# Performance work log

Measured on AMD Instinct MI355X. Metric: run time of the kernel, lower is better.

## Reference

```python
import jax, jax.numpy as jnp
import numpy as np

N_NODES = 100000
N_EDGES = 1600000
D_IN, D_HID, D_OUT = 128, 128, 40


def _degrees(src, dst, n):
    ones = jnp.ones((src.shape[0],), dtype=jnp.float32)
    out_deg = jax.ops.segment_sum(ones, src, num_segments=n)
    in_deg = jax.ops.segment_sum(ones, dst, num_segments=n)
    # DGL clamps zero degrees to 1 to avoid inf
    return jnp.maximum(out_deg, 1.0), jnp.maximum(in_deg, 1.0)


def _graph_conv(x, W, b, src, dst, out_norm, in_norm, n):
    # norm='both': h = D_in^{-1/2} * A^T * (D_out^{-1/2} * x W) + b
    h = x @ W                      # [N, d_out] (W applied first: d_in >= d_out)
    h = h * out_norm[:, None]      # scale source features
    agg = jax.ops.segment_sum(h[src], dst, num_segments=n)  # gather-scatter SpMM
    return agg * in_norm[:, None] + b


def setup_inputs() -> dict:
    key = jax.random.key(0)
    ks = jax.random.split(key, 8)
    x = jax.random.normal(ks[0], (N_NODES, D_IN), dtype=jnp.float32)
    edge_index = jax.random.randint(ks[1], (2, N_EDGES), 0, N_NODES, dtype=jnp.int32)
    def glorot(k, fan_in, fan_out):
        lim = np.sqrt(6.0 / (fan_in + fan_out)).astype(np.float32)
        return jax.random.uniform(k, (fan_in, fan_out), jnp.float32, -lim, lim)
    return {
        "x": x,
        "edge_index": edge_index,
        "W1": glorot(ks[2], D_IN, D_HID), "b1": jnp.zeros((D_HID,), jnp.float32),
        "W2": glorot(ks[3], D_HID, D_HID), "b2": jnp.zeros((D_HID,), jnp.float32),
        "W3": glorot(ks[4], D_HID, D_OUT), "b3": jnp.zeros((D_OUT,), jnp.float32),
    }


def reference(x, edge_index, W1, b1, W2, b2, W3, b3):
    src, dst = edge_index[0], edge_index[1]
    out_deg, in_deg = _degrees(src, dst, N_NODES)
    out_norm = jax.lax.rsqrt(out_deg)
    in_norm = jax.lax.rsqrt(in_deg)
    h = _graph_conv(x, W1, b1, src, dst, out_norm, in_norm, N_NODES)
    h = jax.nn.relu(h)  # dropout inactive at inference
    h = _graph_conv(h, W2, b2, src, dst, out_norm, in_norm, N_NODES)
    h = jax.nn.relu(h)
    h = _graph_conv(h, W3, b3, src, dst, out_norm, in_norm, N_NODES)
    return jax.nn.log_softmax(h, axis=-1)
```

## Files before the change

### kernel.cpp

```cpp
#include <hip/hip_runtime.h>
#include <hip/hip_bf16.h>
#include <math.h>

typedef __hip_bfloat16 bf16;
typedef __attribute__((ext_vector_type(8))) short short8v;
typedef __attribute__((ext_vector_type(4))) float f32x4;

#define ELLW 64
#define NPB 256
#define NBMAX 512
#define CAPB 8192
#define CHUNKA 4096

__device__ __forceinline__ float bflo(unsigned u) { return __uint_as_float(u << 16); }
__device__ __forceinline__ float bfhi(unsigned u) { return __uint_as_float(u & 0xffff0000u); }
__device__ __forceinline__ unsigned short f2bf(float f) {
    unsigned u = __float_as_uint(f);
    return (unsigned short)((u + 0x7fff + ((u >> 16) & 1)) >> 16);
}


__global__ void bucket_scatter(const int* __restrict__ src, const int* __restrict__ dst,
                               int nbk, int* __restrict__ gCurD, int* __restrict__ gCurS,
                               unsigned* __restrict__ pairD, int* __restrict__ srcS, int E) {
    __shared__ int histD[NBMAX], histS[NBMAX], offD[NBMAX], offS[NBMAX];
    int tid = threadIdx.x;
    int base = blockIdx.x * CHUNKA;
    int cnt = E - base; if (cnt > CHUNKA) cnt = CHUNKA;
    for (int i = tid; i < nbk; i += 256) { histD[i] = 0; histS[i] = 0; }
    __syncthreads();
    int sv[16], dv[16];
#pragma unroll
    for (int j = 0; j < 16; ++j) {
        int idx = tid + j * 256;
        if (idx < cnt) {
            sv[j] = src[base + idx];
            dv[j] = dst[base + idx];
            atomicAdd(&histD[dv[j] >> 8], 1);
            atomicAdd(&histS[sv[j] >> 8], 1);
        } else sv[j] = -1;
    }
    __syncthreads();
    for (int i = tid; i < nbk; i += 256) {
        offD[i] = atomicAdd(&gCurD[i], histD[i]);
        offS[i] = atomicAdd(&gCurS[i], histS[i]);
    }
    __syncthreads();
    for (int i = tid; i < nbk; i += 256) { histD[i] = 0; histS[i] = 0; }
    __syncthreads();
#pragma unroll
    for (int j = 0; j < 16; ++j) {
        if (sv[j] >= 0) {
            int bd = dv[j] >> 8;
            int p = atomicAdd(&histD[bd], 1) + offD[bd];
            if (p < CAPB)
                pairD[(size_t)bd * CAPB + p] = ((unsigned)(dv[j] & 255) << 17) | (unsigned)sv[j];
            int bs = sv[j] >> 8;
            int q = atomicAdd(&histS[bs], 1) + offS[bs];
            if (q < CAPB) srcS[(size_t)bs * CAPB + q] = sv[j];
        }
    }
}

__global__ void norm_kernel(const int* __restrict__ cnt_out, const int* __restrict__ cnt_in,
                            float* __restrict__ outn, float* __restrict__ innf, int n) {
    int i = blockIdx.x * blockDim.x + threadIdx.x;
    if (i < n) {
        outn[i] = rsqrtf(fmaxf((float)cnt_out[i], 1.0f));
        innf[i] = rsqrtf(fmaxf((float)cnt_in[i], 1.0f));
    }
}


__device__ __forceinline__ void pack_one(const float* __restrict__ W, bf16* __restrict__ Wb,
                                         int idx, int NOUT, int NPAD) {
    int r = idx & 7;
    int rest = idx >> 3;
    int col = rest % NPAD;
    int sk = rest / NPAD;
    int k = sk * 8 + r;
    float v = (col < NOUT) ? W[k * NOUT + col] : 0.0f;
    Wb[idx] = __float2bfloat16(v);
}

__global__ void pack_all(const float* __restrict__ W1, const float* __restrict__ W2,
                         const float* __restrict__ W3, bf16* __restrict__ Wb1,
                         bf16* __restrict__ Wb2, bf16* __restrict__ Wb3) {
    int idx = blockIdx.x * blockDim.x + threadIdx.x;
    if (idx < 16384) pack_one(W1, Wb1, idx, 128, 128);
    else if (idx < 32768) pack_one(W2, Wb2, idx - 16384, 128, 128);
    else if (idx < 40960) pack_one(W3, Wb3, idx - 32768, 40, 64);
}


template <int NT>
__device__ void gemm_body_f32(int bid, const float* __restrict__ Af,
                              const bf16* __restrict__ Wb, bf16* __restrict__ H, int n) {
    constexpr int NPAD = NT * 16;
    int lane = threadIdx.x & 63;
    int wid = threadIdx.x >> 6;
    int base = (bid * 4 + wid) * 16;
    if (base >= n) return;
    int m = lane & 15, kb = lane >> 4;
    int arow = base + m;

    short8v az = {0, 0, 0, 0, 0, 0, 0, 0};
    short8v a[4];
    const float4* apf = (const float4*)(Af + (size_t)arow * 128);
#pragma unroll
    for (int s = 0; s < 4; ++s) {
        short8v w = az;
        if (arow < n) {
            float4 p = apf[s * 8 + kb * 2];
            float4 q = apf[s * 8 + kb * 2 + 1];
            w[0] = (short)f2bf(p.x); w[1] = (short)f2bf(p.y);
            w[2] = (short)f2bf(p.z); w[3] = (short)f2bf(p.w);
            w[4] = (short)f2bf(q.x); w[5] = (short)f2bf(q.y);
            w[6] = (short)f2bf(q.z); w[7] = (short)f2bf(q.w);
        }
        a[s] = w;
    }

    f32x4 zz = {0.f, 0.f, 0.f, 0.f};
    f32x4 acc[NT];
#pragma unroll
    for (int t = 0; t < NT; ++t) acc[t] = zz;

    const short8v* bp = (const short8v*)Wb;
#pragma unroll
    for (int s = 0; s < 4; ++s) {
#pragma unroll
        for (int t = 0; t < NT; ++t) {
            short8v b = bp[(size_t)(s * 4 + kb) * NPAD + t * 16 + m];
            acc[t] = __builtin_amdgcn_mfma_f32_16x16x32_bf16(a[s], b, acc[t], 0, 0, 0);
        }
    }

    int orow0 = base + kb * 4;
#pragma unroll
    for (int r = 0; r < 4; ++r) {
        int rr = orow0 + r;
        if (rr < n) {
#pragma unroll
            for (int t = 0; t < NT; ++t)
                H[(size_t)rr * NPAD + t * 16 + m] = __float2bfloat16(acc[t][r]);
        }
    }
}


__global__ void phase2(const unsigned* __restrict__ pairD, const int* __restrict__ srcS,
                       const int* __restrict__ gCurD, const int* __restrict__ gCurS,
                       int* __restrict__ ell, int* __restrict__ cnt_in, int* __restrict__ cnt_out,
                       int nbk, int n,
                       const float* __restrict__ x, const bf16* __restrict__ Wb1,
                       bf16* __restrict__ H) {
    int bid = blockIdx.x;
    int tid = threadIdx.x;
    if (bid < nbk) {
        __shared__ int cnt[NPB];
        cnt[tid & (NPB - 1)] = 0;
        __syncthreads();
        int m = gCurD[bid]; if (m > CAPB) m = CAPB;
        const unsigned* p = pairD + (size_t)bid * CAPB;
        int nb0 = bid << 8;
        for (int i = tid; i < m; i += 256) {
            unsigned v = p[i];
            int local = (int)(v >> 17);
            int s = (int)(v & 0x1FFFF);
            int pos = atomicAdd(&cnt[local], 1);
            if (pos < ELLW) ell[((size_t)(nb0 + local) << 6) + pos] = s;
        }
        __syncthreads();
        int node = nb0 + tid;
        if (tid < NPB && node < n) cnt_in[node] = cnt[tid];
    } else if (bid < 2 * nbk) {
        int b = bid - nbk;
        __shared__ int cnt2[NPB];
        cnt2[tid & (NPB - 1)] = 0;
        __syncthreads();
        int m = gCurS[b]; if (m > CAPB) m = CAPB;
        const int* p = srcS + (size_t)b * CAPB;
        int nb0 = b << 8;
        for (int i = tid; i < m; i += 256)
            atomicAdd(&cnt2[p[i] - nb0], 1);
        __syncthreads();
        int node = nb0 + tid;
        if (tid < NPB && node < n) cnt_out[node] = cnt2[tid];
    } else {
        gemm_body_f32<8>(bid - 2 * nbk, x, Wb1, H, n);
    }
}


template <int NT>
__global__ void gather_gemm_fused(const bf16* __restrict__ h, const int* __restrict__ cnt_in,
                                  const int* __restrict__ ell, const float* __restrict__ outn,
                                  const float* __restrict__ inn, const float* __restrict__ bias,
                                  const bf16* __restrict__ Wb, bf16* __restrict__ H, int n) {
    constexpr int NPAD = NT * 16;
    constexpr int NTW = NT / 4;
    __shared__ short rows[16][136];
    int lane = threadIdx.x & 63;
    int wid = threadIdx.x >> 6;
    int nodeBase = blockIdx.x * 16;
    const unsigned* hu = (const unsigned*)h;

#pragma unroll
    for (int q = 0; q < 4; ++q) {
        int r = wid * 4 + q;
        int node = nodeBase + r;
        unsigned pk = 0;
        if (node < n) {
            int d = min(cnt_in[node], ELLW);
            const int* row = ell + (size_t)node * ELLW;
            float a0 = 0.f, a1 = 0.f, a2 = 0.f, a3 = 0.f;
            float a4 = 0.f, a5 = 0.f, a6 = 0.f, a7 = 0.f;
            int k = 0;
            for (; k + 7 < d; k += 8) {
                int e0 = row[k],     e1 = row[k + 1], e2 = row[k + 2], e3 = row[k + 3];
                int e4 = row[k + 4], e5 = row[k + 5], e6 = row[k + 6], e7 = row[k + 7];
                unsigned u0 = hu[(size_t)e0 * 64 + lane];
                unsigned u1 = hu[(size_t)e1 * 64 + lane];
                unsigned u2 = hu[(size_t)e2 * 64 + lane];
                unsigned u3 = hu[(size_t)e3 * 64 + lane];
                unsigned u4 = hu[(size_t)e4 * 64 + lane];
                unsigned u5 = hu[(size_t)e5 * 64 + lane];
                unsigned u6 = hu[(size_t)e6 * 64 + lane];
                unsigned u7 = hu[(size_t)e7 * 64 + lane];
                float o0 = outn[e0], o1 = outn[e1], o2 = outn[e2], o3 = outn[e3];
                float o4 = outn[e4], o5 = outn[e5], o6 = outn[e6], o7 = outn[e7];
                a0 += o0 * bflo(u0); a1 += o0 * bfhi(u0);
                a2 += o1 * bflo(u1); a3 += o1 * bfhi(u1);
                a4 += o2 * bflo(u2); a5 += o2 * bfhi(u2);
                a6 += o3 * bflo(u3); a7 += o3 * bfhi(u3);
                a0 += o4 * bflo(u4); a1 += o4 * bfhi(u4);
                a2 += o5 * bflo(u5); a3 += o5 * bfhi(u5);
                a4 += o6 * bflo(u6); a5 += o6 * bfhi(u6);
                a6 += o7 * bflo(u7); a7 += o7 * bfhi(u7);
            }
            for (; k + 3 < d; k += 4) {
                int e0 = row[k], e1 = row[k + 1], e2 = row[k + 2], e3 = row[k + 3];
                unsigned u0 = hu[(size_t)e0 * 64 + lane];
                unsigned u1 = hu[(size_t)e1 * 64 + lane];
                unsigned u2 = hu[(size_t)e2 * 64 + lane];
                unsigned u3 = hu[(size_t)e3 * 64 + lane];
                float o0 = outn[e0], o1 = outn[e1], o2 = outn[e2], o3 = outn[e3];
                a0 += o0 * bflo(u0); a1 += o0 * bfhi(u0);
                a2 += o1 * bflo(u1); a3 += o1 * bfhi(u1);
                a4 += o2 * bflo(u2); a5 += o2 * bfhi(u2);
                a6 += o3 * bflo(u3); a7 += o3 * bfhi(u3);
            }
            for (; k < d; ++k) {
                int e = row[k];
                unsigned u = hu[(size_t)e * 64 + lane];
                float o = outn[e];
                a0 += o * bflo(u); a1 += o * bfhi(u);
            }
            float innv = inn[node];
            float2 bb = ((const float2*)bias)[lane];
            float f0 = fmaxf(((a0 + a2) + (a4 + a6)) * innv + bb.x, 0.0f);
            float f1 = fmaxf(((a1 + a3) + (a5 + a7)) * innv + bb.y, 0.0f);
            pk = (unsigned)f2bf(f0) | ((unsigned)f2bf(f1) << 16);
        }
        ((unsigned*)rows[r])[lane] = pk;
    }
    __syncthreads();

    int m = lane & 15, kb = lane >> 4;
    short8v a[4];
#pragma unroll
    for (int s = 0; s < 4; ++s)
        a[s] = *(const short8v*)&rows[m][s * 32 + kb * 8];

    f32x4 zz = {0.f, 0.f, 0.f, 0.f};
    f32x4 acc[NTW];
#pragma unroll
    for (int t = 0; t < NTW; ++t) acc[t] = zz;

    const short8v* bp = (const short8v*)Wb;
#pragma unroll
    for (int s = 0; s < 4; ++s) {
#pragma unroll
        for (int t = 0; t < NTW; ++t) {
            int tt = wid * NTW + t;
            short8v b = bp[(size_t)(s * 4 + kb) * NPAD + tt * 16 + m];
            acc[t] = __builtin_amdgcn_mfma_f32_16x16x32_bf16(a[s], b, acc[t], 0, 0, 0);
        }
    }

    int orow0 = nodeBase + kb * 4;
#pragma unroll
    for (int r = 0; r < 4; ++r) {
        int rr = orow0 + r;
        if (rr < n) {
#pragma unroll
            for (int t = 0; t < NTW; ++t)
                H[(size_t)rr * NPAD + (wid * NTW + t) * 16 + m] = __float2bfloat16(acc[t][r]);
        }
    }
}


__global__ void gather40_lsm_p64(const bf16* __restrict__ h, const int* __restrict__ cnt_in,
                                 const int* __restrict__ ell, const float* __restrict__ outn,
                                 const float* __restrict__ inn, const float* __restrict__ b,
                                 float* __restrict__ out, int n) {
    int node = blockIdx.x * 4 + (threadIdx.x >> 6);
    int lane = threadIdx.x & 63;
    if (node >= n) return;
    int d = min(cnt_in[node], ELLW);
    const int* row = ell + (size_t)node * ELLW;
    int grp = lane >> 5;
    int l = lane & 31;
    const unsigned* hu = (const unsigned*)h;
    float a0 = 0.f, a1 = 0.f, a2 = 0.f, a3 = 0.f;
    int k = grp;
    for (; k + 6 < d; k += 8) {
        int e0 = row[k], e1 = row[k + 2], e2 = row[k + 4], e3 = row[k + 6];
        unsigned u0 = hu[(size_t)e0 * 32 + l];
        unsigned u1 = hu[(size_t)e1 * 32 + l];
        unsigned u2 = hu[(size_t)e2 * 32 + l];
        unsigned u3 = hu[(size_t)e3 * 32 + l];
        float o0 = outn[e0], o1 = outn[e1], o2 = outn[e2], o3 = outn[e3];
        a0 += o0 * bflo(u0); a1 += o0 * bfhi(u0);
        a2 += o1 * bflo(u1); a3 += o1 * bfhi(u1);
        a0 += o2 * bflo(u2); a1 += o2 * bfhi(u2);
        a2 += o3 * bflo(u3); a3 += o3 * bfhi(u3);
    }
    for (; k + 2 < d; k += 4) {
        int e0 = row[k], e1 = row[k + 2];
        unsigned u0 = hu[(size_t)e0 * 32 + l];
        unsigned u1 = hu[(size_t)e1 * 32 + l];
        float o0 = outn[e0], o1 = outn[e1];
        a0 += o0 * bflo(u0); a1 += o0 * bfhi(u0);
        a2 += o1 * bflo(u1); a3 += o1 * bfhi(u1);
    }
    if (k < d) {
        int e = row[k];
        unsigned u = hu[(size_t)e * 32 + l];
        float o = outn[e];
        a0 += o * bflo(u); a1 += o * bfhi(u);
    }
    a0 += a2; a1 += a3;
    a0 += __shfl_xor(a0, 32);
    a1 += __shfl_xor(a1, 32);
    float innv = inn[node];
    bool act = (l < 20);
    float2 bb = act ? ((const float2*)b)[l] : make_float2(0.f, 0.f);
    float v0 = act ? (a0 * innv + bb.x) : -INFINITY;
    float v1 = act ? (a1 * innv + bb.y) : -INFINITY;
    float m = fmaxf(v0, v1);
#pragma unroll
    for (int o = 16; o; o >>= 1) m = fmaxf(m, __shfl_xor(m, o));
    float e = act ? (expf(v0 - m) + expf(v1 - m)) : 0.0f;
#pragma unroll
    for (int o = 16; o; o >>= 1) e += __shfl_xor(e, o);
    float ls = m + logf(e);
    if (act && grp == 0)
        ((float2*)(out + (size_t)node * 40))[l] = make_float2(v0 - ls, v1 - ls);
}


extern "C" void kernel_launch(void* const* d_in, const int* in_sizes, int n_in,
                              void* d_out, int out_size, void* d_ws, size_t ws_size,
                              hipStream_t stream) {
    const float* x  = (const float*)d_in[0];
    const int*   ei = (const int*)d_in[1];
    const float* W1 = (const float*)d_in[2];
    const float* b1 = (const float*)d_in[3];
    const float* W2 = (const float*)d_in[4];
    const float* b2 = (const float*)d_in[5];
    const float* W3 = (const float*)d_in[6];
    const float* b3 = (const float*)d_in[7];

    const int n = in_sizes[0] / 128;
    const int E = in_sizes[1] / 2;
    const int* src = ei;
    const int* dst = ei + E;
    const int nbk = (n + NPB - 1) / NPB;

    char* wsb = (char*)d_ws;
    size_t off = 0;
    auto alloc = [&](size_t bytes) { void* p = wsb + off; off = (off + bytes + 63) & ~(size_t)63; return p; };
    float*    outn    = (float*)alloc((size_t)n * 4);
    float*    innf    = (float*)alloc((size_t)n * 4);
    int*      cnt_out = (int*)alloc((size_t)n * 4);
    int*      cnt_in  = (int*)alloc((size_t)n * 4);
    int*      gCurD   = (int*)alloc((size_t)nbk * 4);
    int*      gCurS   = (int*)alloc((size_t)nbk * 4);
    int*      ell     = (int*)alloc((size_t)n * ELLW * 4);
    unsigned* pairD   = (unsigned*)alloc((size_t)nbk * CAPB * 4);
    bf16*     Wb1     = (bf16*)alloc(16 * 128 * 8 * 2);
    bf16*     Wb2     = (bf16*)alloc(16 * 128 * 8 * 2);
    bf16*     Wb3     = (bf16*)alloc(16 * 64 * 8 * 2);
    bf16*     hb      = (bf16*)alloc((size_t)n * 128 * 2);
    bf16*     gb      = (bf16*)alloc((size_t)n * 128 * 2);
    int*      srcS    = (int*)gb;

    hipMemsetAsync(gCurD, 0, ((size_t)((char*)gCurS - (char*)gCurD) + (size_t)nbk * 4), stream);

    pack_all<<<(40960 + 255) / 256, 256, 0, stream>>>(W1, W2, W3, Wb1, Wb2, Wb3);

    bucket_scatter<<<(E + CHUNKA - 1) / CHUNKA, 256, 0, stream>>>(src, dst, nbk, gCurD, gCurS,
                                                                  pairD, srcS, E);
    const int gemmBlocks = (n + 63) / 64;
    phase2<<<2 * nbk + gemmBlocks, 256, 0, stream>>>(pairD, srcS, gCurD, gCurS, ell, cnt_in,
                                                     cnt_out, nbk, n, x, Wb1, hb);
    norm_kernel<<<(n + 255) / 256, 256, 0, stream>>>(cnt_out, cnt_in, outn, innf, n);

    const int fblk = (n + 15) / 16;
    gather_gemm_fused<8><<<fblk, 256, 0, stream>>>(hb, cnt_in, ell, outn, innf, b1, Wb2, gb, n);
    gather_gemm_fused<4><<<fblk, 256, 0, stream>>>(gb, cnt_in, ell, outn, innf, b2, Wb3, hb, n);
    gather40_lsm_p64<<<(n + 3) / 4, 256, 0, stream>>>(hb, cnt_in, ell, outn, innf, b3,
                                                      (float*)d_out, n);
}
```

Measured before the change: 277.0 us.

## Fuse scatter with layer-1 GEMM, fold norm into phase2, widen gather unroll

The edge bucket scatter now runs in the same launch as the first dense GEMM, so the two independent jobs overlap, and the degree normalisation is computed directly in phase2, which removes the separate norm kernel and the cnt_out buffer. The gather loops in the fused gather-GEMM kernel now read neighbour indices as int4 and process 16 neighbours per iteration. The final 40-wide gather gets an extra 16-step unrolled loop. These changes cut launch count and raise memory-level parallelism, at the cost of higher register pressure from the wider unrolling.

```diff
diff --git a/kernel.cpp b/kernel.cpp
--- a/kernel.cpp
+++ b/kernel.cpp
@@ -17,58 +17,6 @@
 __device__ __forceinline__ unsigned short f2bf(float f) {
     unsigned u = __float_as_uint(f);
     return (unsigned short)((u + 0x7fff + ((u >> 16) & 1)) >> 16);
-}
-
-
-__global__ void bucket_scatter(const int* __restrict__ src, const int* __restrict__ dst,
-                               int nbk, int* __restrict__ gCurD, int* __restrict__ gCurS,
-                               unsigned* __restrict__ pairD, int* __restrict__ srcS, int E) {
-    __shared__ int histD[NBMAX], histS[NBMAX], offD[NBMAX], offS[NBMAX];
-    int tid = threadIdx.x;
-    int base = blockIdx.x * CHUNKA;
-    int cnt = E - base; if (cnt > CHUNKA) cnt = CHUNKA;
-    for (int i = tid; i < nbk; i += 256) { histD[i] = 0; histS[i] = 0; }
-    __syncthreads();
-    int sv[16], dv[16];
-#pragma unroll
-    for (int j = 0; j < 16; ++j) {
-        int idx = tid + j * 256;
-        if (idx < cnt) {
-            sv[j] = src[base + idx];
-            dv[j] = dst[base + idx];
-            atomicAdd(&histD[dv[j] >> 8], 1);
-            atomicAdd(&histS[sv[j] >> 8], 1);
-        } else sv[j] = -1;
-    }
-    __syncthreads();
-    for (int i = tid; i < nbk; i += 256) {
-        offD[i] = atomicAdd(&gCurD[i], histD[i]);
-        offS[i] = atomicAdd(&gCurS[i], histS[i]);
-    }
-    __syncthreads();
-    for (int i = tid; i < nbk; i += 256) { histD[i] = 0; histS[i] = 0; }
-    __syncthreads();
-#pragma unroll
-    for (int j = 0; j < 16; ++j) {
-        if (sv[j] >= 0) {
-            int bd = dv[j] >> 8;
-            int p = atomicAdd(&histD[bd], 1) + offD[bd];
-            if (p < CAPB)
-                pairD[(size_t)bd * CAPB + p] = ((unsigned)(dv[j] & 255) << 17) | (unsigned)sv[j];
-            int bs = sv[j] >> 8;
-            int q = atomicAdd(&histS[bs], 1) + offS[bs];
-            if (q < CAPB) srcS[(size_t)bs * CAPB + q] = sv[j];
-        }
-    }
-}
-
-__global__ void norm_kernel(const int* __restrict__ cnt_out, const int* __restrict__ cnt_in,
-                            float* __restrict__ outn, float* __restrict__ innf, int n) {
-    int i = blockIdx.x * blockDim.x + threadIdx.x;
-    if (i < n) {
-        outn[i] = rsqrtf(fmaxf((float)cnt_out[i], 1.0f));
-        innf[i] = rsqrtf(fmaxf((float)cnt_in[i], 1.0f));
-    }
 }
 
 
@@ -149,12 +97,65 @@
 }
 
 
+__device__ void scatter_body(int bid, const int* __restrict__ src, const int* __restrict__ dst,
+                             int nbk, int* __restrict__ gCurD, int* __restrict__ gCurS,
+                             unsigned* __restrict__ pairD, int* __restrict__ srcS, int E) {
+    __shared__ int histD[NBMAX], histS[NBMAX], offD[NBMAX], offS[NBMAX];
+    int tid = threadIdx.x;
+    int base = bid * CHUNKA;
+    int cnt = E - base; if (cnt > CHUNKA) cnt = CHUNKA;
+    for (int i = tid; i < nbk; i += 256) { histD[i] = 0; histS[i] = 0; }
+    __syncthreads();
+    int sv[16], dv[16];
+#pragma unroll
+    for (int j = 0; j < 16; ++j) {
+        int idx = tid + j * 256;
+        if (idx < cnt) {
+            sv[j] = src[base + idx];
+            dv[j] = dst[base + idx];
+            atomicAdd(&histD[dv[j] >> 8], 1);
+            atomicAdd(&histS[sv[j] >> 8], 1);
+        } else sv[j] = -1;
+    }
+    __syncthreads();
+    for (int i = tid; i < nbk; i += 256) {
+        offD[i] = atomicAdd(&gCurD[i], histD[i]);
+        offS[i] = atomicAdd(&gCurS[i], histS[i]);
+    }
+    __syncthreads();
+    for (int i = tid; i < nbk; i += 256) { histD[i] = 0; histS[i] = 0; }
+    __syncthreads();
+#pragma unroll
+    for (int j = 0; j < 16; ++j) {
+        if (sv[j] >= 0) {
+            int bd = dv[j] >> 8;
+            int p = atomicAdd(&histD[bd], 1) + offD[bd];
+            if (p < CAPB)
+                pairD[(size_t)bd * CAPB + p] = ((unsigned)(dv[j] & 255) << 17) | (unsigned)sv[j];
+            int bs = sv[j] >> 8;
+            int q = atomicAdd(&histS[bs], 1) + offS[bs];
+            if (q < CAPB) srcS[(size_t)bs * CAPB + q] = sv[j];
+        }
+    }
+}
+
+
+__global__ void phase1(const int* __restrict__ src, const int* __restrict__ dst,
+                       int nbk, int* __restrict__ gCurD, int* __restrict__ gCurS,
+                       unsigned* __restrict__ pairD, int* __restrict__ srcS, int E,
+                       int scatterBlocks, const float* __restrict__ x,
+                       const bf16* __restrict__ Wb1, bf16* __restrict__ H, int n) {
+    if ((int)blockIdx.x < scatterBlocks)
+        scatter_body(blockIdx.x, src, dst, nbk, gCurD, gCurS, pairD, srcS, E);
+    else
+        gemm_body_f32<8>(blockIdx.x - scatterBlocks, x, Wb1, H, n);
+}
+
+
 __global__ void phase2(const unsigned* __restrict__ pairD, const int* __restrict__ srcS,
                        const int* __restrict__ gCurD, const int* __restrict__ gCurS,
-                       int* __restrict__ ell, int* __restrict__ cnt_in, int* __restrict__ cnt_out,
-                       int nbk, int n,
-                       const float* __restrict__ x, const bf16* __restrict__ Wb1,
-                       bf16* __restrict__ H) {
+                       int* __restrict__ ell, int* __restrict__ cnt_in,
+                       float* __restrict__ innf, float* __restrict__ outn, int nbk, int n) {
     int bid = blockIdx.x;
     int tid = threadIdx.x;
     if (bid < nbk) {
@@ -173,8 +174,11 @@
         }
         __syncthreads();
         int node = nb0 + tid;
-        if (tid < NPB && node < n) cnt_in[node] = cnt[tid];
-    } else if (bid < 2 * nbk) {
+        if (tid < NPB && node < n) {
+            cnt_in[node] = cnt[tid];
+            innf[node] = rsqrtf(fmaxf((float)cnt[tid], 1.0f));
+        }
+    } else {
         int b = bid - nbk;
         __shared__ int cnt2[NPB];
         cnt2[tid & (NPB - 1)] = 0;
@@ -186,9 +190,8 @@
             atomicAdd(&cnt2[p[i] - nb0], 1);
         __syncthreads();
         int node = nb0 + tid;
-        if (tid < NPB && node < n) cnt_out[node] = cnt2[tid];
-    } else {
-        gemm_body_f32<8>(bid - 2 * nbk, x, Wb1, H, n);
+        if (tid < NPB && node < n)
+            outn[node] = rsqrtf(fmaxf((float)cnt2[tid], 1.0f));
     }
 }
 
@@ -213,54 +216,70 @@
         unsigned pk = 0;
         if (node < n) {
             int d = min(cnt_in[node], ELLW);
-            const int* row = ell + (size_t)node * ELLW;
-            float a0 = 0.f, a1 = 0.f, a2 = 0.f, a3 = 0.f;
-            float a4 = 0.f, a5 = 0.f, a6 = 0.f, a7 = 0.f;
+            const int4* row4 = (const int4*)(ell + ((size_t)node << 6));
+            const int* row = (const int*)row4;
+            float aL[4] = {0.f, 0.f, 0.f, 0.f};
+            float aH[4] = {0.f, 0.f, 0.f, 0.f};
             int k = 0;
+            for (; k + 15 < d; k += 16) {
+                int kq = k >> 2;
+                int4 q0 = row4[kq], q1 = row4[kq + 1], q2 = row4[kq + 2], q3 = row4[kq + 3];
+                int e[16] = {q0.x, q0.y, q0.z, q0.w, q1.x, q1.y, q1.z, q1.w,
+                             q2.x, q2.y, q2.z, q2.w, q3.x, q3.y, q3.z, q3.w};
+                unsigned u[16];
+                float o[16];
+#pragma unroll
+                for (int j = 0; j < 16; ++j) u[j] = hu[((size_t)e[j] << 6) + lane];
+#pragma unroll
+                for (int j = 0; j < 16; ++j) o[j] = outn[e[j]];
+#pragma unroll
+                for (int j = 0; j < 16; ++j) {
+                    aL[j & 3] += o[j] * bflo(u[j]);
+                    aH[j & 3] += o[j] * bfhi(u[j]);
+                }
+            }
             for (; k + 7 < d; k += 8) {
-                int e0 = row[k],     e1 = row[k + 1], e2 = row[k + 2], e3 = row[k + 3];
-                int e4 = row[k + 4], e5 = row[k + 5], e6 = row[k + 6], e7 = row[k + 7];
-                unsigned u0 = hu[(size_t)e0 * 64 + lane];
-                unsigned u1 = hu[(size_t)e1 * 64 + lane];
-                unsigned u2 = hu[(size_t)e2 * 64 + lane];
-                unsigned u3 = hu[(size_t)e3 * 64 + lane];
-                unsigned u4 = hu[(size_t)e4 * 64 + lane];
-                unsigned u5 = hu[(size_t)e5 * 64 + lane];
-                unsigned u6 = hu[(size_t)e6 * 64 + lane];
-                unsigned u7 = hu[(size_t)e7 * 64 + lane];
-                float o0 = outn[e0], o1 = outn[e1], o2 = outn[e2], o3 = outn[e3];
-                float o4 = outn[e4], o5 = outn[e5], o6 = outn[e6], o7 = outn[e7];
-                a0 += o0 * bflo(u0); a1 += o0 * bfhi(u0);
-                a2 += o1 * bflo(u1); a3 += o1 * bfhi(u1);
-                a4 += o2 * bflo(u2); a5 += o2 * bfhi(u2);
-                a6 += o3 * bflo(u3); a7 += o3 * bfhi(u3);
-                a0 += o4 * bflo(u4); a1 += o4 * bfhi(u4);
-                a2 += o5 * bflo(u5); a3 += o5 * bfhi(u5);
-                a4 += o6 * bflo(u6); a5 += o6 * bfhi(u6);
-                a6 += o7 * bflo(u7); a7 += o7 * bfhi(u7);
+                int kq = k >> 2;
+                int4 q0 = row4[kq], q1 = row4[kq + 1];
+                int e[8] = {q0.x, q0.y, q0.z, q0.w, q1.x, q1.y, q1.z, q1.w};
+                unsigned u[8];
+                float o[8];
+#pragma unroll
+                for (int j = 0; j < 8; ++j) u[j] = hu[((size_t)e[j] << 6) + lane];
+#pragma unroll
+                for (int j = 0; j < 8; ++j) o[j] = outn[e[j]];
+#pragma unroll
+                for (int j = 0; j < 8; ++j) {
+                    aL[j & 3] += o[j] * bflo(u[j]);
+                    aH[j & 3] += o[j] * bfhi(u[j]);
+                }
             }
             for (; k + 3 < d; k += 4) {
-                int e0 = row[k], e1 = row[k + 1], e2 = row[k + 2], e3 = row[k + 3];
-                unsigned u0 = hu[(size_t)e0 * 64 + lane];
-                unsigned u1 = hu[(size_t)e1 * 64 + lane];
-                unsigned u2 = hu[(size_t)e2 * 64 + lane];
-                unsigned u3 = hu[(size_t)e3 * 64 + lane];
-                float o0 = outn[e0], o1 = outn[e1], o2 = outn[e2], o3 = outn[e3];
-                a0 += o0 * bflo(u0); a1 += o0 * bfhi(u0);
-                a2 += o1 * bflo(u1); a3 += o1 * bfhi(u1);
-                a4 += o2 * bflo(u2); a5 += o2 * bfhi(u2);
-                a6 += o3 * bflo(u3); a7 += o3 * bfhi(u3);
+                int4 q0 = row4[k >> 2];
+                int e[4] = {q0.x, q0.y, q0.z, q0.w};
+                unsigned u[4];
+                float o[4];
+#pragma unroll
+                for (int j = 0; j < 4; ++j) u[j] = hu[((size_t)e[j] << 6) + lane];
+#pragma unroll
+                for (int j = 0; j < 4; ++j) o[j] = outn[e[j]];
+#pragma unroll
+                for (int j = 0; j < 4; ++j) {
+                    aL[j] += o[j] * bflo(u[j]);
+                    aH[j] += o[j] * bfhi(u[j]);
+                }
             }
             for (; k < d; ++k) {
                 int e = row[k];
-                unsigned u = hu[(size_t)e * 64 + lane];
+                unsigned u = hu[((size_t)e << 6) + lane];
                 float o = outn[e];
-                a0 += o * bflo(u); a1 += o * bfhi(u);
+                aL[0] += o * bflo(u);
+                aH[0] += o * bfhi(u);
             }
             float innv = inn[node];
             float2 bb = ((const float2*)bias)[lane];
-            float f0 = fmaxf(((a0 + a2) + (a4 + a6)) * innv + bb.x, 0.0f);
-            float f1 = fmaxf(((a1 + a3) + (a5 + a7)) * innv + bb.y, 0.0f);
+            float f0 = fmaxf(((aL[0] + aL[1]) + (aL[2] + aL[3])) * innv + bb.x, 0.0f);
+            float f1 = fmaxf(((aH[0] + aH[1]) + (aH[2] + aH[3])) * innv + bb.y, 0.0f);
             pk = (unsigned)f2bf(f0) | ((unsigned)f2bf(f1) << 16);
         }
         ((unsigned*)rows[r])[lane] = pk;
@@ -310,18 +329,40 @@
     int lane = threadIdx.x & 63;
     if (node >= n) return;
     int d = min(cnt_in[node], ELLW);
-    const int* row = ell + (size_t)node * ELLW;
+    const int* row = ell + ((size_t)node << 6);
     int grp = lane >> 5;
     int l = lane & 31;
     const unsigned* hu = (const unsigned*)h;
     float a0 = 0.f, a1 = 0.f, a2 = 0.f, a3 = 0.f;
     int k = grp;
+    for (; k + 14 < d; k += 16) {
+        int e0 = row[k],      e1 = row[k + 2],  e2 = row[k + 4],  e3 = row[k + 6];
+        int e4 = row[k + 8],  e5 = row[k + 10], e6 = row[k + 12], e7 = row[k + 14];
+        unsigned u0 = hu[((size_t)e0 << 5) + l];
+        unsigned u1 = hu[((size_t)e1 << 5) + l];
+        unsigned u2 = hu[((size_t)e2 << 5) + l];
+        unsigned u3 = hu[((size_t)e3 << 5) + l];
+        unsigned u4 = hu[((size_t)e4 << 5) + l];
+        unsigned u5 = hu[((size_t)e5 << 5) + l];
+        unsigned u6 = hu[((size_t)e6 << 5) + l];
+        unsigned u7 = hu[((size_t)e7 << 5) + l];
+        float o0 = outn[e0], o1 = outn[e1], o2 = outn[e2], o3 = outn[e3];
+        float o4 = outn[e4], o5 = outn[e5], o6 = outn[e6], o7 = outn[e7];
+        a0 += o0 * bflo(u0); a1 += o0 * bfhi(u0);
+        a2 += o1 * bflo(u1); a3 += o1 * bfhi(u1);
+        a0 += o2 * bflo(u2); a1 += o2 * bfhi(u2);
+        a2 += o3 * bflo(u3); a3 += o3 * bfhi(u3);
+        a0 += o4 * bflo(u4); a1 += o4 * bfhi(u4);
+        a2 += o5 * bflo(u5); a3 += o5 * bfhi(u5);
+        a0 += o6 * bflo(u6); a1 += o6 * bfhi(u6);
+        a2 += o7 * bflo(u7); a3 += o7 * bfhi(u7);
+    }
     for (; k + 6 < d; k += 8) {
         int e0 = row[k], e1 = row[k + 2], e2 = row[k + 4], e3 = row[k + 6];
-        unsigned u0 = hu[(size_t)e0 * 32 + l];
-        unsigned u1 = hu[(size_t)e1 * 32 + l];
-        unsigned u2 = hu[(size_t)e2 * 32 + l];
-        unsigned u3 = hu[(size_t)e3 * 32 + l];
+        unsigned u0 = hu[((size_t)e0 << 5) + l];
+        unsigned u1 = hu[((size_t)e1 << 5) + l];
+        unsigned u2 = hu[((size_t)e2 << 5) + l];
+        unsigned u3 = hu[((size_t)e3 << 5) + l];
         float o0 = outn[e0], o1 = outn[e1], o2 = outn[e2], o3 = outn[e3];
         a0 += o0 * bflo(u0); a1 += o0 * bfhi(u0);
         a2 += o1 * bflo(u1); a3 += o1 * bfhi(u1);
@@ -330,15 +371,15 @@
     }
     for (; k + 2 < d; k += 4) {
         int e0 = row[k], e1 = row[k + 2];
-        unsigned u0 = hu[(size_t)e0 * 32 + l];
-        unsigned u1 = hu[(size_t)e1 * 32 + l];
+        unsigned u0 = hu[((size_t)e0 << 5) + l];
+        unsigned u1 = hu[((size_t)e1 << 5) + l];
         float o0 = outn[e0], o1 = outn[e1];
         a0 += o0 * bflo(u0); a1 += o0 * bfhi(u0);
         a2 += o1 * bflo(u1); a3 += o1 * bfhi(u1);
     }
     if (k < d) {
         int e = row[k];
-        unsigned u = hu[(size_t)e * 32 + l];
+        unsigned u = hu[((size_t)e << 5) + l];
         float o = outn[e];
         a0 += o * bflo(u); a1 += o * bfhi(u);
     }
@@ -385,7 +426,6 @@
     auto alloc = [&](size_t bytes) { void* p = wsb + off; off = (off + bytes + 63) & ~(size_t)63; return p; };
     float*    outn    = (float*)alloc((size_t)n * 4);
     float*    innf    = (float*)alloc((size_t)n * 4);
-    int*      cnt_out = (int*)alloc((size_t)n * 4);
     int*      cnt_in  = (int*)alloc((size_t)n * 4);
     int*      gCurD   = (int*)alloc((size_t)nbk * 4);
     int*      gCurS   = (int*)alloc((size_t)nbk * 4);
@@ -402,12 +442,12 @@
 
     pack_all<<<(40960 + 255) / 256, 256, 0, stream>>>(W1, W2, W3, Wb1, Wb2, Wb3);
 
-    bucket_scatter<<<(E + CHUNKA - 1) / CHUNKA, 256, 0, stream>>>(src, dst, nbk, gCurD, gCurS,
-                                                                  pairD, srcS, E);
+    const int scatterBlocks = (E + CHUNKA - 1) / CHUNKA;
     const int gemmBlocks = (n + 63) / 64;
-    phase2<<<2 * nbk + gemmBlocks, 256, 0, stream>>>(pairD, srcS, gCurD, gCurS, ell, cnt_in,
-                                                     cnt_out, nbk, n, x, Wb1, hb);
-    norm_kernel<<<(n + 255) / 256, 256, 0, stream>>>(cnt_out, cnt_in, outn, innf, n);
+    phase1<<<scatterBlocks + gemmBlocks, 256, 0, stream>>>(src, dst, nbk, gCurD, gCurS, pairD,
+                                                           srcS, E, scatterBlocks, x, Wb1, hb, n);
+    phase2<<<2 * nbk, 256, 0, stream>>>(pairD, srcS, gCurD, gCurS, ell, cnt_in, innf, outn,
+                                        nbk, n);
 
     const int fblk = (n + 15) / 16;
     gather_gemm_fused<8><<<fblk, 256, 0, stream>>>(hb, cnt_in, ell, outn, innf, b1, Wb2, gb, n);
```

After: 289.3 us. +4.4%, slower.
